# Performance work log

Measured on AMD Instinct MI355X. Metric: run time of the kernel, lower is better.

## Reference

```python
import jax, jax.numpy as jnp
import numpy as np
from functools import partial

B, C, COND, L_MEL, HOP, UP = 4, 32, 80, 2048, 8, 8
LAYERS, K, HID, KPK, EMB = 4, 3, 64, 3, 512
L_AUD = L_MEL * UP  # 16384


def conv1d(x, w, b=None, padding=0, dilation=1):
    # x: (B, Cin, L), w: (Cout, Cin, K) -- PyTorch Conv1d semantics
    out = jax.lax.conv_general_dilated(
        x, w, window_strides=(1,), padding=[(padding, padding)],
        rhs_dilation=(dilation,), dimension_numbers=('NCH', 'OIH', 'NCH'))
    if b is not None:
        out = out + b[None, :, None]
    return out


def conv_transpose1d(x, w, stride, pad):
    # PyTorch ConvTranspose1d, weight (Cin, Cout, K), no bias, output_padding=0
    k = w.shape[-1]
    w_eq = jnp.flip(w, -1).transpose(1, 0, 2)  # (Cout, Cin, K)
    lo = k - 1 - pad
    return jax.lax.conv_general_dilated(
        x, w_eq, window_strides=(1,), padding=[(lo, lo)],
        lhs_dilation=(stride,), dimension_numbers=('NCH', 'OIH', 'NCH'))


def lrelu(x, s):
    return jnp.where(x >= 0, x, s * x)


def kernel_predictor(cond, kp_in_w, kp_in_b, kp_res_w1, kp_res_b1,
                     kp_res_w2, kp_res_b2, kp_k_w, kp_k_b, kp_b_w, kp_b_b):
    # FastDiff/UnivNet KernelPredictor: input conv (k=5) + 3 residual blocks + heads
    h = lrelu(conv1d(cond, kp_in_w, kp_in_b, padding=2), 0.1)
    for i in range(3):  # fixed small structural loop
        r = lrelu(conv1d(h, kp_res_w1[i], kp_res_b1[i], padding=1), 0.1)
        r = lrelu(conv1d(r, kp_res_w2[i], kp_res_b2[i], padding=1), 0.1)
        h = h + r
    bsz, _, ln = cond.shape
    k = conv1d(h, kp_k_w, kp_k_b, padding=1)
    b = conv1d(h, kp_b_w, kp_b_b, padding=1)
    kernels = k.reshape(bsz, LAYERS, C, 2 * C, K, ln)
    bias = b.reshape(bsz, LAYERS, 2 * C, ln)
    return kernels, bias


def location_variable_convolution(x, kernel, bias, dilation, hop):
    # x: (B, Cin, L), kernel: (B, Cin, Cout, K, Lf), bias: (B, Cout, Lf)
    bsz, cin, ln = x.shape
    _, _, cout, ks, lf = kernel.shape
    pad = dilation * (ks - 1) // 2
    xp = jnp.pad(x, ((0, 0), (0, 0), (pad, pad)))
    # gather per-frame sliding windows: (Lf, hop, K)
    pos = (jnp.arange(lf) * hop)[:, None, None] \
        + jnp.arange(hop)[None, :, None] \
        + (jnp.arange(ks) * dilation)[None, None, :]
    xw = xp[:, :, pos]  # (B, Cin, Lf, hop, K)
    o = jnp.einsum('bilsk,biokl->bols', xw, kernel)  # (B, Cout, Lf, hop)
    o = o + bias[:, :, :, None]
    return o.reshape(bsz, cout, lf * hop)


def forward(x, audio_down, c, noise_embedding, fc_t_w, fc_t_b, up_w, conv_w,
            kp_in_w, kp_in_b, kp_res_w1, kp_res_b1, kp_res_w2, kp_res_b2,
            kp_k_w, kp_k_b, kp_b_w, kp_b_b):
    noise = (noise_embedding @ fc_t_w.T + fc_t_b)[:, :, None]  # (B, 80, 1)
    condition = c + noise
    kernels, bias = kernel_predictor(condition, kp_in_w, kp_in_b, kp_res_w1,
                                     kp_res_b1, kp_res_w2, kp_res_b2,
                                     kp_k_w, kp_k_b, kp_b_w, kp_b_b)
    h = lrelu(x, 0.2)
    h = conv_transpose1d(h, up_w, UP, UP // 2)  # (B, 32, 16384)
    for i in range(LAYERS):
        h = h + audio_down
        y = lrelu(h, 0.2)
        y = conv1d(y, conv_w[i], padding=3 ** i, dilation=3 ** i)
        y = lrelu(y, 0.2)
        y = location_variable_convolution(y, kernels[:, i], bias[:, i], 1, HOP)
        h = h + jax.nn.sigmoid(y[:, :C, :]) * jnp.tanh(y[:, C:, :])
    return h


def setup_inputs() -> dict:
    key = jax.random.key(0)
    ks = jax.random.split(key, 20)
    s = 0.02
    kch = LAYERS * C * (2 * C) * K  # 24576
    bch = LAYERS * 2 * C            # 256
    return {
        'x': jax.random.normal(ks[0], (B, C, L_MEL), jnp.float32),
        'audio_down': jax.random.normal(ks[1], (B, C, L_AUD), jnp.float32),
        'c': jax.random.normal(ks[2], (B, COND, L_MEL), jnp.float32),
        'noise_embedding': jax.random.normal(ks[3], (B, EMB), jnp.float32),
        'fc_t_w': jax.random.normal(ks[4], (COND, EMB), jnp.float32) * s,
        'fc_t_b': jnp.zeros((COND,), jnp.float32),
        'up_w': jax.random.normal(ks[5], (C, C, UP * 2), jnp.float32) * s,
        'conv_w': jax.random.normal(ks[6], (LAYERS, C, C, K), jnp.float32) * s,
        'kp_in_w': jax.random.normal(ks[7], (HID, COND, 5), jnp.float32) * s,
        'kp_in_b': jnp.zeros((HID,), jnp.float32),
        'kp_res_w1': jax.random.normal(ks[8], (3, HID, HID, KPK), jnp.float32) * s,
        'kp_res_b1': jnp.zeros((3, HID), jnp.float32),
        'kp_res_w2': jax.random.normal(ks[9], (3, HID, HID, KPK), jnp.float32) * s,
        'kp_res_b2': jnp.zeros((3, HID), jnp.float32),
        'kp_k_w': jax.random.normal(ks[10], (kch, HID, KPK), jnp.float32) * s,
        'kp_k_b': jnp.zeros((kch,), jnp.float32),
        'kp_b_w': jax.random.normal(ks[11], (bch, HID, KPK), jnp.float32) * s,
        'kp_b_b': jnp.zeros((bch,), jnp.float32),
    }


def reference(x, audio_down, c, noise_embedding, fc_t_w, fc_t_b, up_w, conv_w,
              kp_in_w, kp_in_b, kp_res_w1, kp_res_b1, kp_res_w2, kp_res_b2,
              kp_k_w, kp_k_b, kp_b_w, kp_b_b):
    return forward(x, audio_down, c, noise_embedding, fc_t_w, fc_t_b, up_w,
                   conv_w, kp_in_w, kp_in_b, kp_res_w1, kp_res_b1, kp_res_w2,
                   kp_res_b2, kp_k_w, kp_k_b, kp_b_w, kp_b_b)
```

## Files before the change

kernel.cpp:

```cpp
#include <hip/hip_runtime.h>
#include <math.h>

#define B_      4
#define C_      32
#define COND_   80
#define LMEL_   2048
#define HOP_    8
#define UP_     8
#define LAYERS_ 4
#define K_      3
#define HID_    64
#define KPK_    3
#define EMB_    512
#define LAUD_   (LMEL_*UP_)
#define KCH_    (LAYERS_*C_*2*C_*K_)
#define BCH_    (LAYERS_*2*C_)
#define Y2S     (LAUD_ + 8)

typedef short v8s __attribute__((ext_vector_type(8)));
typedef float v4f __attribute__((ext_vector_type(4)));

__device__ __forceinline__ float lrelu_(float v, float s) { return v >= 0.f ? v : s * v; }

__device__ __forceinline__ unsigned short f2bf(float f) {
  unsigned int x = __float_as_uint(f);
  unsigned int r = (x + 0x7FFFu + ((x >> 16) & 1u)) >> 16;
  return (unsigned short)r;
}

#define GLOAD16(GSRC, LDST)                                              \
  __builtin_amdgcn_global_load_lds(                                     \
      (const __attribute__((address_space(1))) unsigned int*)(GSRC),    \
      (__attribute__((address_space(3))) unsigned int*)(LDST), 16, 0, 0)

#define WAITV(N) asm volatile("s_waitcnt vmcnt(" #N ")" ::: "memory")

__global__ void k_mkWTs(const float* __restrict__ src, float* __restrict__ dst,
                        int S, int OC, int ICK) {
  int idx = blockIdx.x*256 + threadIdx.x;
  if (idx >= S*OC*ICK) return;
  int s = idx / (OC*ICK), rem = idx % (OC*ICK);
  int oc = rem / ICK, ick = rem % ICK;
  dst[s*OC*ICK + ick*OC + oc] = src[idx];
}

__global__ void k_noise_cond(const float* __restrict__ ne, const float* __restrict__ fw,
                             const float* __restrict__ fb, const float* __restrict__ c,
                             float* __restrict__ cond) {
  int b = blockIdx.x / COND_;
  int cc = blockIdx.x % COND_;
  __shared__ float red[256];
  float p = 0.f;
  for (int j = threadIdx.x; j < EMB_; j += 256)
    p += ne[b*EMB_ + j] * fw[cc*EMB_ + j];
  red[threadIdx.x] = p;
  __syncthreads();
  for (int s = 128; s > 0; s >>= 1) {
    if (threadIdx.x < s) red[threadIdx.x] += red[threadIdx.x + s];
    __syncthreads();
  }
  float noise = red[0] + fb[cc];
  const float* cp = c + (b*COND_ + cc)*LMEL_;
  float* op = cond + (b*COND_ + cc)*LMEL_;
  for (int l = threadIdx.x; l < LMEL_; l += 256) op[l] = cp[l] + noise;
}

__global__ __launch_bounds__(256) void k_kp_in(const float* __restrict__ cond, const float* __restrict__ wT,
                                               const float* __restrict__ bias, float* __restrict__ out) {
  const int T = 32;
  int b  = blockIdx.x / (LMEL_/T);
  int lb = (blockIdx.x % (LMEL_/T)) * T;
  __shared__ float sc[COND_][T + 4];
  for (int idx = threadIdx.x; idx < COND_*(T+4); idx += 256) {
    int cc = idx / (T+4), j = idx % (T+4);
    int l = lb + j - 2;
    sc[cc][j] = (l >= 0 && l < LMEL_) ? cond[(b*COND_ + cc)*LMEL_ + l] : 0.f;
  }
  __syncthreads();
  int ch = threadIdx.x & 63;
  int lq = threadIdx.x >> 6;
  float acc[8];
#pragma unroll
  for (int ii = 0; ii < 8; ii++) acc[ii] = bias[ch];
  for (int cc = 0; cc < COND_; cc++) {
    float r[12];
#pragma unroll
    for (int j = 0; j < 12; j++) r[j] = sc[cc][lq*8 + j];
#pragma unroll
    for (int k = 0; k < 5; k++) {
      float wv = wT[(cc*5 + k)*64 + ch];
#pragma unroll
      for (int ii = 0; ii < 8; ii++) acc[ii] = fmaf(wv, r[ii + k], acc[ii]);
    }
  }
  float* op = out + (b*HID_ + ch)*LMEL_ + lb + lq*8;
#pragma unroll
  for (int ii = 0; ii < 8; ii++) acc[ii] = lrelu_(acc[ii], 0.1f);
  *reinterpret_cast<float4*>(&op[0]) = make_float4(acc[0], acc[1], acc[2], acc[3]);
  *reinterpret_cast<float4*>(&op[4]) = make_float4(acc[4], acc[5], acc[6], acc[7]);
}

__global__ __launch_bounds__(256) void k_kp_res2(const float* __restrict__ in,
                                                 const float* __restrict__ w1T, const float* __restrict__ b1,
                                                 const float* __restrict__ w2T, const float* __restrict__ b2,
                                                 float* __restrict__ out) {
  const int T = 32;
  int b  = blockIdx.x / (LMEL_/T);
  int lb = (blockIdx.x % (LMEL_/T)) * T;
  __shared__ float si[HID_][38];
  __shared__ float sr[HID_][38];
  for (int idx = threadIdx.x; idx < HID_*36; idx += 256) {
    int cc = idx / 36, j = idx % 36;
    int l = lb - 2 + j;
    si[cc][j] = (l >= 0 && l < LMEL_) ? in[(b*HID_ + cc)*LMEL_ + l] : 0.f;
  }
  __syncthreads();
  int ch = threadIdx.x & 63;
  int lq = threadIdx.x >> 6;
  {
    float b1v = b1[ch];
    float a1[9];
#pragma unroll
    for (int jj = 0; jj < 9; jj++) a1[jj] = b1v;
    for (int cc = 0; cc < HID_; cc++) {
      float r[11];
#pragma unroll
      for (int j = 0; j < 11; j++) r[j] = si[cc][lq*9 + j];
#pragma unroll
      for (int k = 0; k < 3; k++) {
        float wv = w1T[(cc*3 + k)*64 + ch];
#pragma unroll
        for (int jj = 0; jj < 9; jj++) a1[jj] = fmaf(wv, r[jj + k], a1[jj]);
      }
    }
#pragma unroll
    for (int jj = 0; jj < 9; jj++) {
      int m = lq*9 + jj;
      if (m < 34) sr[ch][m] = lrelu_(a1[jj], 0.1f);
    }
  }
  __syncthreads();
  {
    float b2v = b2[ch];
    float a2[8];
#pragma unroll
    for (int jj = 0; jj < 8; jj++) a2[jj] = b2v;
    for (int cc = 0; cc < HID_; cc++) {
      float r[10];
#pragma unroll
      for (int j = 0; j < 10; j++) r[j] = sr[cc][lq*8 + j];
#pragma unroll
      for (int k = 0; k < 3; k++) {
        float wv = w2T[(cc*3 + k)*64 + ch];
#pragma unroll
        for (int jj = 0; jj < 8; jj++) a2[jj] = fmaf(wv, r[jj + k], a2[jj]);
      }
    }
    float* op = out + (b*HID_ + ch)*LMEL_ + lb + lq*8;
    float v[8];
#pragma unroll
    for (int jj = 0; jj < 8; jj++)
      v[jj] = si[ch][lq*8 + jj + 2] + lrelu_(a2[jj], 0.1f);
    *reinterpret_cast<float4*>(&op[0]) = make_float4(v[0], v[1], v[2], v[3]);
    *reinterpret_cast<float4*>(&op[4]) = make_float4(v[4], v[5], v[6], v[7]);
  }
}

__global__ __launch_bounds__(256) void k_kp_bias(const float* __restrict__ in, const float* __restrict__ wT,
                                                 const float* __restrict__ bias, float* __restrict__ out) {
  const int T = 16;
  int b  = blockIdx.x / (LMEL_/T);
  int lb = (blockIdx.x % (LMEL_/T)) * T;
  __shared__ float si[HID_][T + 2];
  for (int idx = threadIdx.x; idx < HID_*(T+2); idx += 256) {
    int cc = idx / (T+2), j = idx % (T+2);
    int l = lb + j - 1;
    si[cc][j] = (l >= 0 && l < LMEL_) ? in[(b*HID_ + cc)*LMEL_ + l] : 0.f;
  }
  __syncthreads();
  int ch = threadIdx.x;
  float acc[T];
  float bv = bias[ch];
#pragma unroll
  for (int ii = 0; ii < T; ii++) acc[ii] = bv;
  for (int cc = 0; cc < HID_; cc++) {
    float w0 = wT[(cc*3 + 0)*256 + ch];
    float w1 = wT[(cc*3 + 1)*256 + ch];
    float w2 = wT[(cc*3 + 2)*256 + ch];
#pragma unroll
    for (int ii = 0; ii < T; ii++)
      acc[ii] = fmaf(w0, si[cc][ii], fmaf(w1, si[cc][ii+1], fmaf(w2, si[cc][ii+2], acc[ii])));
  }
  float* op = out + (b*BCH_ + ch)*LMEL_ + lb;
#pragma unroll
  for (int q = 0; q < 4; q++)
    *reinterpret_cast<float4*>(&op[q*4]) = make_float4(acc[q*4], acc[q*4+1], acc[q*4+2], acc[q*4+3]);
}

__global__ void k_mkUp(const float* __restrict__ upw, float* __restrict__ wt) {
  int idx = blockIdx.x*256 + threadIdx.x;
  if (idx >= C_*C_*16) return;
  int co = idx & 31, j = (idx >> 5) & 15, ci = idx >> 9;
  wt[idx] = upw[(ci*C_ + co)*16 + j];
}

#define UT 32
__global__ __launch_bounds__(256) void k_upsample(const float* __restrict__ x, const float* __restrict__ wt,
                                                  float* __restrict__ h) {
  int b  = blockIdx.x / 65;
  int s0 = (blockIdx.x % 65) * UT;
  __shared__ float sw[16384];
  __shared__ float sx[C_][33 + 3];
  for (int idx = threadIdx.x*4; idx < 16384; idx += 1024)
    *reinterpret_cast<float4*>(&sw[idx]) = *reinterpret_cast<const float4*>(&wt[idx]);
  for (int idx = threadIdx.x; idx < C_*33; idx += 256) {
    int ci = idx / 33, i = idx % 33;
    int s = s0 - 1 + i;
    float v = (s >= 0 && s < LMEL_) ? x[(b*C_ + ci)*LMEL_ + s] : 0.f;
    sx[ci][i] = lrelu_(v, 0.2f);
  }
  __syncthreads();
  int co = threadIdx.x & 31, sq = threadIdx.x >> 5;
  float acc[4][8];
#pragma unroll
  for (int k = 0; k < 4; k++)
#pragma unroll
    for (int r = 0; r < 8; r++) acc[k][r] = 0.f;
  for (int ci = 0; ci < C_; ci++) {
    float xv[5];
#pragma unroll
    for (int m = 0; m < 5; m++) xv[m] = sx[ci][sq*4 + m];
    const float* wl = &sw[ci*512 + co];
#pragma unroll
    for (int r = 0; r < 8; r++) {
      float wa = wl[r*32];
      float wb = wl[(r+8)*32];
#pragma unroll
      for (int k = 0; k < 4; k++)
        acc[k][r] = fmaf(wa, xv[k+1], fmaf(wb, xv[k], acc[k][r]));
    }
  }
  float* op = h + ((size_t)b*C_ + co)*LAUD_;
#pragma unroll
  for (int k = 0; k < 4; k++) {
    int s1 = s0 + sq*4 + k;
    int lo = 8*s1 - 4;
    if (lo >= 0 && lo + 4 <= LAUD_)
      *reinterpret_cast<float4*>(&op[lo]) = make_float4(acc[k][0], acc[k][1], acc[k][2], acc[k][3]);
    if (lo >= -4 && lo + 8 <= LAUD_)
      *reinterpret_cast<float4*>(&op[lo+4]) = make_float4(acc[k][4], acc[k][5], acc[k][6], acc[k][7]);
  }
}

__global__ void k_mkA(const float* __restrict__ kw, unsigned short* __restrict__ waf) {
  int idx = blockIdx.x*256 + threadIdx.x;
  if (idx >= KCH_*HID_*KPK_) return;
  int i    = idx & 7;
  int lane = (idx >> 3) & 63;
  int ks   = (idx >> 9) % 6;
  int tile = (idx / 3072) & 3;
  int rk   = idx / 12288;
  int layer = rk / 96, rem = rk % 96, ci = rem / 3, kk = rem % 3;
  int cout = tile*16 + (lane & 15);
  int j    = ks*32 + ((lane >> 4) << 3) + i;
  int row  = ((layer*32 + ci)*64 + cout)*3 + kk;
  waf[idx] = f2bf(kw[row*192 + j]);
}

__global__ void k_mkKbT(const float* __restrict__ kb, float* __restrict__ kbt) {
  int idx = blockIdx.x*256 + threadIdx.x;
  if (idx >= KCH_) return;
  int cr = idx & 15, tile = (idx >> 4) & 3, rk = idx >> 6;
  int layer = rk / 96, rem = rk % 96, ci = rem / 3, kk = rem % 3;
  int cout = tile*16 + cr;
  kbt[idx] = kb[((layer*32 + ci)*64 + cout)*3 + kk];
}

template<int DIL>
__global__ __launch_bounds__(256) void k_dilconv(const float* __restrict__ h, const float* __restrict__ ad,
                                                 const float* __restrict__ wT, float* __restrict__ y2p) {
  const int T = 128;
  int b  = blockIdx.x / (LAUD_/T);
  int tb = (blockIdx.x % (LAUD_/T)) * T;
  const int W = T + 2*DIL;
  __shared__ float ss[C_][T + 2*27 + 4];
  for (int idx = threadIdx.x; idx < C_*W; idx += 256) {
    int ci = idx / W, j = idx % W;
    int t = tb - DIL + j;
    float v = 0.f;
    if (t >= 0 && t < LAUD_) {
      int g = (b*C_ + ci)*LAUD_ + t;
      v = h[g] + ad[g];
    }
    ss[ci][j] = lrelu_(v, 0.2f);
  }
  if (tb == 0 && threadIdx.x < 128) {
    int ci = threadIdx.x >> 2, q = threadIdx.x & 3;
    y2p[(size_t)(b*C_ + ci)*Y2S + q] = 0.f;
  }
  if (tb == LAUD_ - T && threadIdx.x < 128) {
    int ci = threadIdx.x >> 2, q = threadIdx.x & 3;
    y2p[(size_t)(b*C_ + ci)*Y2S + 4 + LAUD_ + q] = 0.f;
  }
  __syncthreads();
  int co = threadIdx.x & 31, tq = threadIdx.x >> 5;
  float acc[16];
#pragma unroll
  for (int ii = 0; ii < 16; ii++) acc[ii] = 0.f;
  for (int ci = 0; ci < C_; ci++) {
    float w0 = wT[(ci*3 + 0)*32 + co];
    float w1 = wT[(ci*3 + 1)*32 + co];
    float w2 = wT[(ci*3 + 2)*32 + co];
#pragma unroll
    for (int ii = 0; ii < 16; ii++) {
      int tl = tq*16 + ii;
      acc[ii] = fmaf(w0, ss[ci][tl], fmaf(w1, ss[ci][tl + DIL], fmaf(w2, ss[ci][tl + 2*DIL], acc[ii])));
    }
  }
  float* op = y2p + (size_t)(b*C_ + co)*Y2S + 4 + tb + tq*16;
#pragma unroll
  for (int ii = 0; ii < 16; ii++) acc[ii] = lrelu_(acc[ii], 0.2f);
#pragma unroll
  for (int q = 0; q < 4; q++)
    *reinterpret_cast<float4*>(&op[q*4]) = make_float4(acc[q*4], acc[q*4+1], acc[q*4+2], acc[q*4+3]);
}

#define STAGE(BUF, STEP)                                                         \
  {                                                                              \
    const unsigned short* gsrc = waf + (size_t)((layer*96 + (STEP))*4)*3072;     \
    { int u = tid; int tpx = (u >= 384); int wi = u - tpx*384;                   \
      GLOAD16(gsrc + (v + 2*tpx)*3072 + wi*8,                                    \
              (char*)stg + (BUF)*12288 + u*16); }                                \
    if (tid < 256) { int u = tid + 512; int wi = u - 384;                        \
      GLOAD16(gsrc + (v + 2)*3072 + wi*8, (char*)stg + (BUF)*12288 + u*16); }    \
  }

__global__ __launch_bounds__(512, 2) void k_lvc_mfma(
    const float* __restrict__ hkp, const unsigned short* __restrict__ waf,
    const float* __restrict__ kbt, const float* __restrict__ biasb,
    const float* __restrict__ y2p, const float* __restrict__ ad,
    float* __restrict__ h, int layer) {
  int b  = blockIdx.x >> 6;
  int r6 = blockIdx.x & 63;
  int l0 = (r6 >> 1) * 64;
  int v  = r6 & 1;

  __shared__ __align__(16) char pool[152064];
  unsigned short* stg   = (unsigned short*)pool;
  unsigned short* FB    = (unsigned short*)(pool + 49152);
  float*          kbt_s = (float*)(pool + 73728);
  float*          sy    = (float*)(pool + 86016);
  float*          shh   = (float*)pool;
  float*          red   = (float*)pool;

  int tid = threadIdx.x;
  {
    const float* ysrc = y2p + (size_t)(b*C_)*Y2S + 4 + (size_t)l0*8 - 1;
    for (int idx = tid; idx < 32*514; idx += 512) {
      int ci = idx / 514, j = idx % 514;
      sy[ci*516 + j] = ysrc[(size_t)ci*Y2S + j];
    }
  }
  for (int u = tid; u < 3072; u += 512) {
    int step = u >> 5, tp2 = (u >> 4) & 1, cr = u & 15;
    kbt_s[u] = kbt[((layer*96 + step)*4 + v + 2*tp2)*16 + cr];
  }
  for (int idx = tid; idx < HID_*66; idx += 512) {
    int hh = idx / 66, j = idx % 66;
    int l = l0 - 1 + j;
    shh[hh*66 + j] = (l >= 0 && l < LMEL_) ? hkp[(b*HID_ + hh)*LMEL_ + l] : 0.f;
  }
  __syncthreads();
  for (int u = tid; u < 12288; u += 512) {
    int i = u & 7, lane2 = (u >> 3) & 63, ksf = u >> 9;
    int ks = ksf % 6, fg2 = ksf / 6;
    int k = ks*32 + ((lane2 >> 4) << 3) + i;
    int col = lane2 & 15;
    int hh = k / 3, q = k - hh*3;
    FB[u] = f2bf(shh[hh*66 + fg2*16 + col + q]);
  }
  __syncthreads();

  int wave = tid >> 6, lane = tid & 63;
  int tp = wave & 1, fg = wave >> 1;
  int f = lane & 15;
  const int kbl = ((lane >> 4) << 2);

  v8s bfr[6];
#pragma unroll
  for (int ks = 0; ks < 6; ks++)
    bfr[ks] = *reinterpret_cast<const v8s*>(&FB[((fg*6 + ks)*64 + lane)*8]);

  float o[4][8];
#pragma unroll
  for (int r = 0; r < 4; r++)
#pragma unroll
    for (int s = 0; s < 8; s++) o[r][s] = 0.f;

  STAGE(0, 0)
  STAGE(1, 1)
  if (wave < 4) { WAITV(2); } else { WAITV(1); }
  __builtin_amdgcn_s_barrier();

  const int sybase = (fg*16 + f)*8;

  for (int ci = 0; ci < 32; ci++) {
    float syr[12];
    {
      const float* yrow = sy + ci*516 + sybase;
      float4 q0 = *reinterpret_cast<const float4*>(yrow);
      float4 q1 = *reinterpret_cast<const float4*>(yrow + 4);
      float4 q2 = *reinterpret_cast<const float4*>(yrow + 8);
      syr[0]=q0.x; syr[1]=q0.y; syr[2]=q0.z; syr[3]=q0.w;
      syr[4]=q1.x; syr[5]=q1.y; syr[6]=q1.z; syr[7]=q1.w;
      syr[8]=q2.x; syr[9]=q2.y; syr[10]=q2.z; syr[11]=q2.w;
    }
#pragma unroll
    for (int kk = 0; kk < 3; kk++) {
      int step = ci*3 + kk;
      if (step < 94) {
        STAGE((step + 2) & 3, step + 2)
        if (wave < 4) { WAITV(2); } else { WAITV(1); }
      } else {
        WAITV(0);
      }
      __builtin_amdgcn_s_barrier();

      const unsigned short* sa = stg + (step & 3)*6144 + tp*3072;
      v4f acc = {0.f, 0.f, 0.f, 0.f};
#pragma unroll
      for (int ks = 0; ks < 6; ks++) {
        v8s a = *reinterpret_cast<const v8s*>(sa + ks*512 + lane*8);
        acc = __builtin_amdgcn_mfma_f32_16x16x32_bf16(a, bfr[ks], acc, 0, 0, 0);
      }
      float4 kb4 = *reinterpret_cast<const float4*>(&kbt_s[(step*2 + tp)*16 + kbl]);
#pragma unroll
      for (int r = 0; r < 4; r++) {
        float kern = acc[r] + ((const float*)&kb4)[r];
#pragma unroll
        for (int s = 0; s < 8; s++)
          o[r][s] = fmaf(kern, syr[kk + s], o[r][s]);
      }
    }
  }

#pragma unroll
  for (int r = 0; r < 4; r++) {
    int cout = (v + 2*tp)*16 + kbl + r;
    float bv = biasb[((size_t)b*BCH_ + layer*2*C_ + cout)*LMEL_ + l0 + fg*16 + f];
#pragma unroll
    for (int s = 0; s < 8; s++) o[r][s] += bv;
  }
  if (tp == 1) {
#pragma unroll
    for (int r = 0; r < 4; r++)
#pragma unroll
      for (int s = 0; s < 8; s++)
        red[(fg*64 + lane)*33 + r*8 + s] = o[r][s];
  }
  __syncthreads();
  if (tp == 0) {
#pragma unroll
    for (int r = 0; r < 4; r++) {
      int cout = v*16 + kbl + r;
      size_t base = ((size_t)b*C_ + cout)*LAUD_ + (size_t)(l0 + fg*16 + f)*HOP_;
      float4 h0 = *reinterpret_cast<const float4*>(&h[base]);
      float4 h1 = *reinterpret_cast<const float4*>(&h[base + 4]);
      float4 a0 = *reinterpret_cast<const float4*>(&ad[base]);
      float4 a1 = *reinterpret_cast<const float4*>(&ad[base + 4]);
      float outv[8];
#pragma unroll
      for (int s = 0; s < 8; s++) {
        float vv = o[r][s];
        float tv = red[(fg*64 + lane)*33 + r*8 + s];
        float sig = 1.f / (1.f + __expf(-vv));
        float th  = 1.f - 2.f / (1.f + __expf(2.f*tv));
        float hv = (s < 4) ? ((const float*)&h0)[s] : ((const float*)&h1)[s-4];
        float av = (s < 4) ? ((const float*)&a0)[s] : ((const float*)&a1)[s-4];
        outv[s] = hv + av + sig * th;
      }
      *reinterpret_cast<float4*>(&h[base])     = make_float4(outv[0], outv[1], outv[2], outv[3]);
      *reinterpret_cast<float4*>(&h[base + 4]) = make_float4(outv[4], outv[5], outv[6], outv[7]);
    }
  }
}

extern "C" void kernel_launch(void* const* d_in, const int* in_sizes, int n_in,
                              void* d_out, int out_size, void* d_ws, size_t ws_size,
                              hipStream_t stream) {
  const float* x     = (const float*)d_in[0];
  const float* ad    = (const float*)d_in[1];
  const float* c     = (const float*)d_in[2];
  const float* ne    = (const float*)d_in[3];
  const float* fw    = (const float*)d_in[4];
  const float* fb    = (const float*)d_in[5];
  const float* upw   = (const float*)d_in[6];
  const float* convw = (const float*)d_in[7];
  const float* kinw  = (const float*)d_in[8];
  const float* kinb  = (const float*)d_in[9];
  const float* krw1  = (const float*)d_in[10];
  const float* krb1  = (const float*)d_in[11];
  const float* krw2  = (const float*)d_in[12];
  const float* krb2  = (const float*)d_in[13];
  const float* kkw   = (const float*)d_in[14];
  const float* kkb   = (const float*)d_in[15];
  const float* kbw   = (const float*)d_in[16];
  const float* kbb   = (const float*)d_in[17];
  float* h = (float*)d_out;

  float* ws = (float*)d_ws;
  float* cond   = ws; ws += B_*COND_*LMEL_;
  float* hkpa   = ws; ws += B_*HID_*LMEL_;
  float* hkpb   = ws; ws += B_*HID_*LMEL_;
  float* biasb  = ws; ws += B_*BCH_*LMEL_;
  float* y2p    = ws; ws += B_*C_*Y2S;
  float* kbt    = ws; ws += KCH_;
  float* wtup   = ws; ws += C_*C_*16;
  float* kinwT  = ws; ws += HID_*COND_*5;
  float* krw1T  = ws; ws += 3*HID_*HID_*3;
  float* krw2T  = ws; ws += 3*HID_*HID_*3;
  float* kbwT   = ws; ws += BCH_*HID_*3;
  float* convwT = ws; ws += LAYERS_*C_*C_*3;
  unsigned short* waf = (unsigned short*)ws; ws += (KCH_*HID_*KPK_)/2;

  k_mkA<<<(KCH_*HID_*KPK_ + 255)/256, 256, 0, stream>>>(kkw, waf);
  k_mkKbT<<<(KCH_ + 255)/256, 256, 0, stream>>>(kkb, kbt);
  k_mkUp<<<(C_*C_*16 + 255)/256, 256, 0, stream>>>(upw, wtup);
  k_mkWTs<<<(HID_*COND_*5 + 255)/256, 256, 0, stream>>>(kinw, kinwT, 1, HID_, COND_*5);
  k_mkWTs<<<(3*HID_*HID_*3 + 255)/256, 256, 0, stream>>>(krw1, krw1T, 3, HID_, HID_*3);
  k_mkWTs<<<(3*HID_*HID_*3 + 255)/256, 256, 0, stream>>>(krw2, krw2T, 3, HID_, HID_*3);
  k_mkWTs<<<(BCH_*HID_*3 + 255)/256, 256, 0, stream>>>(kbw, kbwT, 1, BCH_, HID_*3);
  k_mkWTs<<<(LAYERS_*C_*C_*3 + 255)/256, 256, 0, stream>>>(convw, convwT, LAYERS_, C_, C_*3);

  k_noise_cond<<<B_*COND_, 256, 0, stream>>>(ne, fw, fb, c, cond);
  k_kp_in<<<B_*(LMEL_/32), 256, 0, stream>>>(cond, kinwT, kinb, hkpa);
  k_kp_res2<<<B_*(LMEL_/32), 256, 0, stream>>>(hkpa, krw1T + 0*HID_*HID_*3, krb1 + 0*HID_,
                                               krw2T + 0*HID_*HID_*3, krb2 + 0*HID_, hkpb);
  k_kp_res2<<<B_*(LMEL_/32), 256, 0, stream>>>(hkpb, krw1T + 1*HID_*HID_*3, krb1 + 1*HID_,
                                               krw2T + 1*HID_*HID_*3, krb2 + 1*HID_, hkpa);
  k_kp_res2<<<B_*(LMEL_/32), 256, 0, stream>>>(hkpa, krw1T + 2*HID_*HID_*3, krb1 + 2*HID_,
                                               krw2T + 2*HID_*HID_*3, krb2 + 2*HID_, hkpb);
  k_kp_bias<<<B_*(LMEL_/16), 256, 0, stream>>>(hkpb, kbwT, kbb, biasb);
  k_upsample<<<B_*65, 256, 0, stream>>>(x, wtup, h);

  for (int i = 0; i < LAYERS_; i++) {
    const float* wci = convwT + i*C_*C_*3;
    switch (i) {
      case 0: k_dilconv<1 ><<<B_*(LAUD_/128), 256, 0, stream>>>(h, ad, wci, y2p); break;
      case 1: k_dilconv<3 ><<<B_*(LAUD_/128), 256, 0, stream>>>(h, ad, wci, y2p); break;
      case 2: k_dilconv<9 ><<<B_*(LAUD_/128), 256, 0, stream>>>(h, ad, wci, y2p); break;
      case 3: k_dilconv<27><<<B_*(LAUD_/128), 256, 0, stream>>>(h, ad, wci, y2p); break;
    }
    k_lvc_mfma<<<B_*64, 512, 0, stream>>>(hkpb, waf, kbt, biasb, y2p, ad, h, i);
  }
}
```

Baseline: 502.6 us.

## Deepen LVC weight staging to five buffers and pad sy rows against bank conflicts

The LVC MFMA kernel's async weight-staging ring grows from 4 to 5 LDS buffers with 4 steps prefetched ahead. Each new load is now issued after the current step's compute, so only one barrier per step guards buffer reuse. The sy row layout is padded (36 floats per 32) to cut LDS bank conflicts on the float4 reads. FB is moved inside the staging region so total LDS shrinks, which adds an extra sync after the bfr preload and needs exact waitcnt bookkeeping in the tail steps.

```diff
diff --git a/kernel.cpp b/kernel.cpp
--- a/kernel.cpp
+++ b/kernel.cpp
@@ -325,14 +325,49 @@
     *reinterpret_cast<float4*>(&op[q*4]) = make_float4(acc[q*4], acc[q*4+1], acc[q*4+2], acc[q*4+3]);
 }
 
+#define SYW(j) ((((j) >> 5) * 36) + ((j) & 31))
+
 #define STAGE(BUF, STEP)                                                         \
   {                                                                              \
     const unsigned short* gsrc = waf + (size_t)((layer*96 + (STEP))*4)*3072;     \
     { int u = tid; int tpx = (u >= 384); int wi = u - tpx*384;                   \
       GLOAD16(gsrc + (v + 2*tpx)*3072 + wi*8,                                    \
-              (char*)stg + (BUF)*12288 + u*16); }                                \
+              (char*)stg + (size_t)(BUF)*12288 + u*16); }                        \
     if (tid < 256) { int u = tid + 512; int wi = u - 384;                        \
-      GLOAD16(gsrc + (v + 2)*3072 + wi*8, (char*)stg + (BUF)*12288 + u*16); }    \
+      GLOAD16(gsrc + (v + 2)*3072 + wi*8,                                        \
+              (char*)stg + (size_t)(BUF)*12288 + u*16); }                        \
+  }
+
+#define LOADSYR(CI)                                                              \
+  float syr[12];                                                                 \
+  {                                                                              \
+    const float* yrow = sy + (CI)*580;                                           \
+    float4 q0 = *reinterpret_cast<const float4*>(yrow + off0);                   \
+    float4 q1 = *reinterpret_cast<const float4*>(yrow + off1);                   \
+    float4 q2 = *reinterpret_cast<const float4*>(yrow + off2);                   \
+    syr[0]=q0.x; syr[1]=q0.y; syr[2]=q0.z; syr[3]=q0.w;                          \
+    syr[4]=q1.x; syr[5]=q1.y; syr[6]=q1.z; syr[7]=q1.w;                          \
+    syr[8]=q2.x; syr[9]=q2.y; syr[10]=q2.z; syr[11]=q2.w;                        \
+  }
+
+#define DOSTEP(CI, KK, ISSUE, WA, WB)                                            \
+  {                                                                              \
+    const int step_ = (CI)*3 + (KK);                                             \
+    const unsigned short* sa = stg + (size_t)(step_ % 5)*6144 + tp*3072;         \
+    v4f acc = {0.f, 0.f, 0.f, 0.f};                                              \
+    _Pragma("unroll") for (int ks = 0; ks < 6; ks++) {                           \
+      v8s a = *reinterpret_cast<const v8s*>(sa + ks*512 + lane*8);               \
+      acc = __builtin_amdgcn_mfma_f32_16x16x32_bf16(a, bfr[ks], acc, 0, 0, 0);   \
+    }                                                                            \
+    float4 kb4 = *reinterpret_cast<const float4*>(&kbt_s[(step_*2 + tp)*16 + kbl]); \
+    _Pragma("unroll") for (int r = 0; r < 4; r++) {                              \
+      float kern = acc[r] + ((const float*)&kb4)[r];                             \
+      _Pragma("unroll") for (int s = 0; s < 8; s++)                              \
+        o[r][s] = fmaf(kern, syr[(KK) + s], o[r][s]);                            \
+    }                                                                            \
+    if ((ISSUE) >= 0) { STAGE(((ISSUE) % 5), (ISSUE)) }                          \
+    if (wave < 4) { WAITV(WA); } else { WAITV(WB); }                             \
+    __builtin_amdgcn_s_barrier();                                                \
   }
 
 __global__ __launch_bounds__(512, 2) void k_lvc_mfma(
@@ -345,12 +380,12 @@
   int l0 = (r6 >> 1) * 64;
   int v  = r6 & 1;
 
-  __shared__ __align__(16) char pool[152064];
+  __shared__ __align__(16) char pool[147968];
   unsigned short* stg   = (unsigned short*)pool;
-  unsigned short* FB    = (unsigned short*)(pool + 49152);
-  float*          kbt_s = (float*)(pool + 73728);
-  float*          sy    = (float*)(pool + 86016);
+  float*          kbt_s = (float*)(pool + 61440);
+  float*          sy    = (float*)(pool + 73728);
   float*          shh   = (float*)pool;
+  unsigned short* FB    = (unsigned short*)(pool + 17408);
   float*          red   = (float*)pool;
 
   int tid = threadIdx.x;
@@ -358,7 +393,7 @@
     const float* ysrc = y2p + (size_t)(b*C_)*Y2S + 4 + (size_t)l0*8 - 1;
     for (int idx = tid; idx < 32*514; idx += 512) {
       int ci = idx / 514, j = idx % 514;
-      sy[ci*516 + j] = ysrc[(size_t)ci*Y2S + j];
+      sy[ci*580 + SYW(j)] = ysrc[(size_t)ci*Y2S + j];
     }
   }
   for (int u = tid; u < 3072; u += 512) {
@@ -390,58 +425,44 @@
 #pragma unroll
   for (int ks = 0; ks < 6; ks++)
     bfr[ks] = *reinterpret_cast<const v8s*>(&FB[((fg*6 + ks)*64 + lane)*8]);
+  asm volatile("s_waitcnt lgkmcnt(0)" ::: "memory");
+  __syncthreads();
 
   float o[4][8];
 #pragma unroll
   for (int r = 0; r < 4; r++)
 #pragma unroll
     for (int s = 0; s < 8; s++) o[r][s] = 0.f;
+
+  const int sybase = (fg*16 + f)*8;
+  const int off0 = SYW(sybase);
+  const int off1 = SYW(sybase + 4);
+  const int off2 = SYW(sybase + 8);
 
   STAGE(0, 0)
   STAGE(1, 1)
-  if (wave < 4) { WAITV(2); } else { WAITV(1); }
+  STAGE(2, 2)
+  STAGE(3, 3)
+  if (wave < 4) { WAITV(6); } else { WAITV(3); }
   __builtin_amdgcn_s_barrier();
 
-  const int sybase = (fg*16 + f)*8;
-
-  for (int ci = 0; ci < 32; ci++) {
-    float syr[12];
-    {
-      const float* yrow = sy + ci*516 + sybase;
-      float4 q0 = *reinterpret_cast<const float4*>(yrow);
-      float4 q1 = *reinterpret_cast<const float4*>(yrow + 4);
-      float4 q2 = *reinterpret_cast<const float4*>(yrow + 8);
-      syr[0]=q0.x; syr[1]=q0.y; syr[2]=q0.z; syr[3]=q0.w;
-      syr[4]=q1.x; syr[5]=q1.y; syr[6]=q1.z; syr[7]=q1.w;
-      syr[8]=q2.x; syr[9]=q2.y; syr[10]=q2.z; syr[11]=q2.w;
-    }
-#pragma unroll
-    for (int kk = 0; kk < 3; kk++) {
-      int step = ci*3 + kk;
-      if (step < 94) {
-        STAGE((step + 2) & 3, step + 2)
-        if (wave < 4) { WAITV(2); } else { WAITV(1); }
-      } else {
-        WAITV(0);
-      }
-      __builtin_amdgcn_s_barrier();
-
-      const unsigned short* sa = stg + (step & 3)*6144 + tp*3072;
-      v4f acc = {0.f, 0.f, 0.f, 0.f};
-#pragma unroll
-      for (int ks = 0; ks < 6; ks++) {
-        v8s a = *reinterpret_cast<const v8s*>(sa + ks*512 + lane*8);
-        acc = __builtin_amdgcn_mfma_f32_16x16x32_bf16(a, bfr[ks], acc, 0, 0, 0);
-      }
-      float4 kb4 = *reinterpret_cast<const float4*>(&kbt_s[(step*2 + tp)*16 + kbl]);
-#pragma unroll
-      for (int r = 0; r < 4; r++) {
-        float kern = acc[r] + ((const float*)&kb4)[r];
-#pragma unroll
-        for (int s = 0; s < 8; s++)
-          o[r][s] = fmaf(kern, syr[kk + s], o[r][s]);
-      }
-    }
+  for (int ci = 0; ci < 30; ci++) {
+    LOADSYR(ci)
+    DOSTEP(ci, 0, ci*3 + 4, 6, 3)
+    DOSTEP(ci, 1, ci*3 + 5, 6, 3)
+    DOSTEP(ci, 2, ci*3 + 6, 6, 3)
+  }
+  {
+    LOADSYR(30)
+    DOSTEP(30, 0, 94, 6, 3)
+    DOSTEP(30, 1, 95, 6, 3)
+    DOSTEP(30, 2, -1, 4, 2)
+  }
+  {
+    LOADSYR(31)
+    DOSTEP(31, 0, -1, 2, 1)
+    DOSTEP(31, 1, -1, 0, 0)
+    DOSTEP(31, 2, -1, 0, 0)
   }
 
 #pragma unroll
```

Measured after the change: 489.4 us. 2.6% less time.

## Split LVC input channels across wave pairs, reuse A tiles across two frame groups

Applied to the files above, without the earlier changes.

Restructures the LVC MFMA kernel so each wave computes two 16-frame groups with one A-fragment load (two MFMAs per load). The 32 input channels are split between two wave halves and combined through a shared-memory reduction at the end. Staging moves to a 3-deep buffer that loads the matching steps for both channel halves at once. The y tile gets a padded, swizzled LDS layout to reduce bank conflicts. This halves the staged weight traffic per output and reduces the number of barrier steps, at the cost of more registers (two accumulator sets) and an extra reduction pass.

```diff
diff --git a/kernel.cpp b/kernel.cpp
--- a/kernel.cpp
+++ b/kernel.cpp
@@ -325,14 +325,60 @@
     *reinterpret_cast<float4*>(&op[q*4]) = make_float4(acc[q*4], acc[q*4+1], acc[q*4+2], acc[q*4+3]);
 }
 
-#define STAGE(BUF, STEP)                                                         \
+#define SYW(j) ((((j) >> 5) * 36) + ((j) & 31))
+
+#define STAGE2(PH)                                                               \
   {                                                                              \
-    const unsigned short* gsrc = waf + (size_t)((layer*96 + (STEP))*4)*3072;     \
-    { int u = tid; int tpx = (u >= 384); int wi = u - tpx*384;                   \
-      GLOAD16(gsrc + (v + 2*tpx)*3072 + wi*8,                                    \
-              (char*)stg + (BUF)*12288 + u*16); }                                \
-    if (tid < 256) { int u = tid + 512; int wi = u - 384;                        \
-      GLOAD16(gsrc + (v + 2)*3072 + wi*8, (char*)stg + (BUF)*12288 + u*16); }    \
+    const size_t rbase = (size_t)(layer*96 + (PH))*4*3072;                       \
+    const size_t rbase2 = (size_t)(layer*96 + 48 + (PH))*4*3072;                 \
+    char* dst = (char*)stg + (size_t)((PH) % 3)*24576;                           \
+    _Pragma("unroll") for (int kq = 0; kq < 3; kq++) {                           \
+      int u = tid + kq*512;                                                      \
+      int seg = u / 384, wi = u - seg*384;                                       \
+      size_t src = (seg < 2 ? rbase : rbase2) + (size_t)(v + 2*(seg & 1))*3072;  \
+      GLOAD16(waf + src + wi*8, dst + u*16);                                     \
+    }                                                                            \
+  }
+
+#define LOADSYR2()                                                               \
+  {                                                                              \
+    const float* yrow = sy + ciw*580;                                            \
+    float4 a0 = *reinterpret_cast<const float4*>(yrow + off00);                  \
+    float4 a1 = *reinterpret_cast<const float4*>(yrow + off01);                  \
+    float4 a2 = *reinterpret_cast<const float4*>(yrow + off02);                  \
+    syr0[0]=a0.x; syr0[1]=a0.y; syr0[2]=a0.z; syr0[3]=a0.w;                      \
+    syr0[4]=a1.x; syr0[5]=a1.y; syr0[6]=a1.z; syr0[7]=a1.w;                      \
+    syr0[8]=a2.x; syr0[9]=a2.y; syr0[10]=a2.z; syr0[11]=a2.w;                    \
+    float4 b0 = *reinterpret_cast<const float4*>(yrow + off10);                  \
+    float4 b1 = *reinterpret_cast<const float4*>(yrow + off11);                  \
+    float4 b2 = *reinterpret_cast<const float4*>(yrow + off12);                  \
+    syr1[0]=b0.x; syr1[1]=b0.y; syr1[2]=b0.z; syr1[3]=b0.w;                      \
+    syr1[4]=b1.x; syr1[5]=b1.y; syr1[6]=b1.z; syr1[7]=b1.w;                      \
+    syr1[8]=b2.x; syr1[9]=b2.y; syr1[10]=b2.z; syr1[11]=b2.w;                    \
+  }
+
+#define DOSTEP2(KK, ISSUE_OK, WN)                                                \
+  {                                                                              \
+    const unsigned short* sa = stg + (size_t)(KK)*12288 + ch*6144 + tp*3072;     \
+    v4f acc0 = {0.f,0.f,0.f,0.f}, acc1 = {0.f,0.f,0.f,0.f};                      \
+    _Pragma("unroll") for (int ks = 0; ks < 6; ks++) {                           \
+      v8s a = *reinterpret_cast<const v8s*>(sa + ks*512 + lane*8);               \
+      acc0 = __builtin_amdgcn_mfma_f32_16x16x32_bf16(a, bfrA[ks], acc0, 0, 0, 0);\
+      acc1 = __builtin_amdgcn_mfma_f32_16x16x32_bf16(a, bfrB[ks], acc1, 0, 0, 0);\
+    }                                                                            \
+    int step_ = ch*48 + cw*3 + (KK);                                             \
+    float4 kb4 = *reinterpret_cast<const float4*>(&kbt_s[(step_*2 + tp)*16 + kbl]); \
+    _Pragma("unroll") for (int r = 0; r < 4; r++) {                              \
+      float k0 = acc0[r] + ((const float*)&kb4)[r];                              \
+      float k1 = acc1[r] + ((const float*)&kb4)[r];                              \
+      _Pragma("unroll") for (int s = 0; s < 8; s++) {                            \
+        o0[r][s] = fmaf(k0, syr0[(KK) + s], o0[r][s]);                           \
+        o1[r][s] = fmaf(k1, syr1[(KK) + s], o1[r][s]);                           \
+      }                                                                          \
+    }                                                                            \
+    if (ISSUE_OK) { STAGE2(cw*3 + (KK) + 2) }                                    \
+    WAITV(WN);                                                                   \
+    __builtin_amdgcn_s_barrier();                                                \
   }
 
 __global__ __launch_bounds__(512, 2) void k_lvc_mfma(
@@ -345,12 +391,12 @@
   int l0 = (r6 >> 1) * 64;
   int v  = r6 & 1;
 
-  __shared__ __align__(16) char pool[152064];
+  __shared__ __align__(16) char pool[160256];
   unsigned short* stg   = (unsigned short*)pool;
-  unsigned short* FB    = (unsigned short*)(pool + 49152);
-  float*          kbt_s = (float*)(pool + 73728);
-  float*          sy    = (float*)(pool + 86016);
+  float*          sy    = (float*)(pool + 73728);
+  float*          kbt_s = (float*)(pool + 147968);
   float*          shh   = (float*)pool;
+  unsigned short* FB    = (unsigned short*)(pool + 16896);
   float*          red   = (float*)pool;
 
   int tid = threadIdx.x;
@@ -358,7 +404,7 @@
     const float* ysrc = y2p + (size_t)(b*C_)*Y2S + 4 + (size_t)l0*8 - 1;
     for (int idx = tid; idx < 32*514; idx += 512) {
       int ci = idx / 514, j = idx % 514;
-      sy[ci*516 + j] = ysrc[(size_t)ci*Y2S + j];
+      sy[ci*580 + SYW(j)] = ysrc[(size_t)ci*Y2S + j];
     }
   }
   for (int u = tid; u < 3072; u += 512) {
@@ -373,114 +419,120 @@
   __syncthreads();
   for (int u = tid; u < 12288; u += 512) {
     int i = u & 7, lane2 = (u >> 3) & 63, ksf = u >> 9;
-    int ks = ksf % 6, fg2 = ksf / 6;
+    int ks = ksf % 6, g2 = ksf / 6;
     int k = ks*32 + ((lane2 >> 4) << 3) + i;
     int col = lane2 & 15;
     int hh = k / 3, q = k - hh*3;
-    FB[u] = f2bf(shh[hh*66 + fg2*16 + col + q]);
+    FB[u] = f2bf(shh[hh*66 + g2*16 + col + q]);
   }
   __syncthreads();
 
   int wave = tid >> 6, lane = tid & 63;
-  int tp = wave & 1, fg = wave >> 1;
+  int tp = wave & 1, ch = (wave >> 1) & 1, fg = wave >> 2;
   int f = lane & 15;
   const int kbl = ((lane >> 4) << 2);
 
-  v8s bfr[6];
-#pragma unroll
-  for (int ks = 0; ks < 6; ks++)
-    bfr[ks] = *reinterpret_cast<const v8s*>(&FB[((fg*6 + ks)*64 + lane)*8]);
-
-  float o[4][8];
+  v8s bfrA[6], bfrB[6];
+#pragma unroll
+  for (int ks = 0; ks < 6; ks++) {
+    bfrA[ks] = *reinterpret_cast<const v8s*>(&FB[(((2*fg)*6 + ks)*64 + lane)*8]);
+    bfrB[ks] = *reinterpret_cast<const v8s*>(&FB[(((2*fg + 1)*6 + ks)*64 + lane)*8]);
+  }
+  asm volatile("s_waitcnt lgkmcnt(0)" ::: "memory");
+  __syncthreads();
+
+  float o0[4][8], o1[4][8];
 #pragma unroll
   for (int r = 0; r < 4; r++)
 #pragma unroll
-    for (int s = 0; s < 8; s++) o[r][s] = 0.f;
-
-  STAGE(0, 0)
-  STAGE(1, 1)
-  if (wave < 4) { WAITV(2); } else { WAITV(1); }
+    for (int s = 0; s < 8; s++) { o0[r][s] = 0.f; o1[r][s] = 0.f; }
+
+  const int sb0 = (fg*32 + f)*8, sb1 = (fg*32 + 16 + f)*8;
+  const int off00 = SYW(sb0), off01 = SYW(sb0+4), off02 = SYW(sb0+8);
+  const int off10 = SYW(sb1), off11 = SYW(sb1+4), off12 = SYW(sb1+8);
+
+  STAGE2(0)
+  STAGE2(1)
+  WAITV(3);
   __builtin_amdgcn_s_barrier();
 
-  const int sybase = (fg*16 + f)*8;
-
-  for (int ci = 0; ci < 32; ci++) {
-    float syr[12];
-    {
-      const float* yrow = sy + ci*516 + sybase;
-      float4 q0 = *reinterpret_cast<const float4*>(yrow);
-      float4 q1 = *reinterpret_cast<const float4*>(yrow + 4);
-      float4 q2 = *reinterpret_cast<const float4*>(yrow + 8);
-      syr[0]=q0.x; syr[1]=q0.y; syr[2]=q0.z; syr[3]=q0.w;
-      syr[4]=q1.x; syr[5]=q1.y; syr[6]=q1.z; syr[7]=q1.w;
-      syr[8]=q2.x; syr[9]=q2.y; syr[10]=q2.z; syr[11]=q2.w;
-    }
-#pragma unroll
-    for (int kk = 0; kk < 3; kk++) {
-      int step = ci*3 + kk;
-      if (step < 94) {
-        STAGE((step + 2) & 3, step + 2)
-        if (wave < 4) { WAITV(2); } else { WAITV(1); }
-      } else {
-        WAITV(0);
+  float syr0[12], syr1[12];
+  for (int cw = 0; cw < 15; cw++) {
+    const int ciw = ch*16 + cw;
+    LOADSYR2()
+    DOSTEP2(0, 1, 3)
+    DOSTEP2(1, 1, 3)
+    DOSTEP2(2, 1, 3)
+  }
+  {
+    const int cw = 15;
+    const int ciw = ch*16 + 15;
+    LOADSYR2()
+    DOSTEP2(0, 1, 3)
+    DOSTEP2(1, 0, 0)
+    DOSTEP2(2, 0, 0)
+  }
+
+#define REDI(FGTP, L, IDX) red[((FGTP)*64 + (L))*65 + (IDX)]
+  if (ch == 1) {
+#pragma unroll
+    for (int r = 0; r < 4; r++)
+#pragma unroll
+      for (int s = 0; s < 8; s++) {
+        REDI(fg*2 + tp, lane, r*8 + s)      = o0[r][s];
+        REDI(fg*2 + tp, lane, 32 + r*8 + s) = o1[r][s];
       }
-      __builtin_amdgcn_s_barrier();
-
-      const unsigned short* sa = stg + (step & 3)*6144 + tp*3072;
-      v4f acc = {0.f, 0.f, 0.f, 0.f};
-#pragma unroll
-      for (int ks = 0; ks < 6; ks++) {
-        v8s a = *reinterpret_cast<const v8s*>(sa + ks*512 + lane*8);
-        acc = __builtin_amdgcn_mfma_f32_16x16x32_bf16(a, bfr[ks], acc, 0, 0, 0);
+  }
+  __syncthreads();
+  if (ch == 0) {
+    int cout = (v + 2*tp)*16 + kbl;
+#pragma unroll
+    for (int r = 0; r < 4; r++) {
+      float bv0 = biasb[((size_t)b*BCH_ + layer*2*C_ + cout + r)*LMEL_ + l0 + fg*32 + f];
+      float bv1 = biasb[((size_t)b*BCH_ + layer*2*C_ + cout + r)*LMEL_ + l0 + fg*32 + 16 + f];
+#pragma unroll
+      for (int s = 0; s < 8; s++) {
+        o0[r][s] += REDI(fg*2 + tp, lane, r*8 + s) + bv0;
+        o1[r][s] += REDI(fg*2 + tp, lane, 32 + r*8 + s) + bv1;
       }
-      float4 kb4 = *reinterpret_cast<const float4*>(&kbt_s[(step*2 + tp)*16 + kbl]);
+    }
+  }
+  __syncthreads();
+  if (ch == 0 && tp == 1) {
+#pragma unroll
+    for (int r = 0; r < 4; r++)
+#pragma unroll
+      for (int s = 0; s < 8; s++) {
+        REDI(fg*2 + 1, lane, r*8 + s)      = o0[r][s];
+        REDI(fg*2 + 1, lane, 32 + r*8 + s) = o1[r][s];
+      }
+  }
+  __syncthreads();
+  if (ch == 0 && tp == 0) {
+#pragma unroll
+    for (int g = 0; g < 2; g++) {
 #pragma unroll
       for (int r = 0; r < 4; r++) {
-        float kern = acc[r] + ((const float*)&kb4)[r];
-#pragma unroll
-        for (int s = 0; s < 8; s++)
-          o[r][s] = fmaf(kern, syr[kk + s], o[r][s]);
+        int cout = v*16 + kbl + r;
+        size_t base = ((size_t)b*C_ + cout)*LAUD_ + (size_t)(l0 + fg*32 + g*16 + f)*HOP_;
+        float4 h0 = *reinterpret_cast<const float4*>(&h[base]);
+        float4 h1 = *reinterpret_cast<const float4*>(&h[base + 4]);
+        float4 a0 = *reinterpret_cast<const float4*>(&ad[base]);
+        float4 a1 = *reinterpret_cast<const float4*>(&ad[base + 4]);
+        float outv[8];
+#pragma unroll
+        for (int s = 0; s < 8; s++) {
+          float vv = g ? o1[r][s] : o0[r][s];
+          float tv = REDI(fg*2 + 1, lane, g*32 + r*8 + s);
+          float sig = 1.f / (1.f + __expf(-vv));
+          float th  = 1.f - 2.f / (1.f + __expf(2.f*tv));
+          float hv = (s < 4) ? ((const float*)&h0)[s] : ((const float*)&h1)[s-4];
+          float av = (s < 4) ? ((const float*)&a0)[s] : ((const float*)&a1)[s-4];
+          outv[s] = hv + av + sig * th;
+        }
+        *reinterpret_cast<float4*>(&h[base])     = make_float4(outv[0], outv[1], outv[2], outv[3]);
+        *reinterpret_cast<float4*>(&h[base + 4]) = make_float4(outv[4], outv[5], outv[6], outv[7]);
       }
-    }
-  }
-
-#pragma unroll
-  for (int r = 0; r < 4; r++) {
-    int cout = (v + 2*tp)*16 + kbl + r;
-    float bv = biasb[((size_t)b*BCH_ + layer*2*C_ + cout)*LMEL_ + l0 + fg*16 + f];
-#pragma unroll
-    for (int s = 0; s < 8; s++) o[r][s] += bv;
-  }
-  if (tp == 1) {
-#pragma unroll
-    for (int r = 0; r < 4; r++)
-#pragma unroll
-      for (int s = 0; s < 8; s++)
-        red[(fg*64 + lane)*33 + r*8 + s] = o[r][s];
-  }
-  __syncthreads();
-  if (tp == 0) {
-#pragma unroll
-    for (int r = 0; r < 4; r++) {
-      int cout = v*16 + kbl + r;
-      size_t base = ((size_t)b*C_ + cout)*LAUD_ + (size_t)(l0 + fg*16 + f)*HOP_;
-      float4 h0 = *reinterpret_cast<const float4*>(&h[base]);
-      float4 h1 = *reinterpret_cast<const float4*>(&h[base + 4]);
-      float4 a0 = *reinterpret_cast<const float4*>(&ad[base]);
-      float4 a1 = *reinterpret_cast<const float4*>(&ad[base + 4]);
-      float outv[8];
-#pragma unroll
-      for (int s = 0; s < 8; s++) {
-        float vv = o[r][s];
-        float tv = red[(fg*64 + lane)*33 + r*8 + s];
-        float sig = 1.f / (1.f + __expf(-vv));
-        float th  = 1.f - 2.f / (1.f + __expf(2.f*tv));
-        float hv = (s < 4) ? ((const float*)&h0)[s] : ((const float*)&h1)[s-4];
-        float av = (s < 4) ? ((const float*)&a0)[s] : ((const float*)&a1)[s-4];
-        outv[s] = hv + av + sig * th;
-      }
-      *reinterpret_cast<float4*>(&h[base])     = make_float4(outv[0], outv[1], outv[2], outv[3]);
-      *reinterpret_cast<float4*>(&h[base + 4]) = make_float4(outv[4], outv[5], outv[6], outv[7]);
     }
   }
 }
```

Result: faster. 460.0 us (-8.5%).
